# Optimization experiments

Measured on AMD Instinct MI355X. Metric: run time of the kernel, lower is better.

## Reference

```python
import math
import jax, jax.numpy as jnp
import numpy as np

ALPHA = 12.0  # agg_alpha
TAU = 0.07


def setup_inputs() -> dict:
    key = jax.random.key(0)
    kq, kk, kqm, kkm = jax.random.split(key, 4)
    B, Lq, O, Lk, D = 64, 32, 128, 256, 128
    q = jax.random.normal(kq, (B, Lq, D), dtype=jnp.float32)
    k = jax.random.normal(kk, (O, Lk, D), dtype=jnp.float32)
    # True = padding token (masked out)
    q_mask = jax.random.bernoulli(kqm, 0.1, (B, Lq))
    k_mask = jax.random.bernoulli(kkm, 0.1, (O, Lk))
    logit_scale = jnp.asarray(math.log(1.0 / TAU), dtype=jnp.float32)
    return {"q": q, "k": k, "q_mask": q_mask, "k_mask": k_mask,
            "logit_scale": logit_scale}


def _l2norm(x, eps=1e-12):
    # torch F.normalize: x / max(||x||_2, eps)
    n = jnp.sqrt(jnp.sum(x * x, axis=-1, keepdims=True))
    return x / jnp.maximum(n, eps)


def reference(q, k, q_mask, k_mask, logit_scale):
    B, Lq, D = q.shape
    O, Lk, _ = k.shape
    qn = _l2norm(q)
    kn = _l2norm(k)
    # S: [B, O, Lq, Lk] full similarity tensor (the kernel-headroom intermediate)
    S = jnp.einsum('bid,ojd->boij', qn, kn)
    m = q_mask[:, None, :, None] | k_mask[None, :, None, :]
    S = jnp.where(m, -jnp.inf, S)
    # softmax-pool over Lk: logsumexp(alpha*S)/alpha, then sum over Lq
    s = jax.nn.logsumexp(ALPHA * S, axis=-1) / ALPHA  # [B, O, Lq]
    s = jnp.sum(s, axis=-1)                            # [B, O]
    s = jnp.where(jnp.isfinite(s), s, jnp.zeros_like(s))
    # length_norm = 'sqrt'
    s = s / (math.sqrt(Lq * Lk) + 1e-06)
    # learnable temperature, exp clamped at 100
    scale = jnp.minimum(jnp.exp(logit_scale), 100.0)
    return s * scale
```

## Files before the change

### kernel.cpp

```cpp
#include <hip/hip_runtime.h>
#include <math.h>


#define ALPHA 12.0f

constexpr int B_  = 64;
constexpr int LQ  = 32;
constexpr int O_  = 128;
constexpr int LK  = 256;
constexpr int LKH = 128;
constexpr int D_  = 128;
constexpr int LDH = D_ + 8;

typedef _Float16 half8   __attribute__((ext_vector_type(8)));
typedef _Float16 half4_t __attribute__((ext_vector_type(4)));
typedef float    f32x4   __attribute__((ext_vector_type(4)));

__global__ __launch_bounds__(256, 1)
void colbert_partial_kernel(const float* __restrict__ q,
                            const float* __restrict__ k,
                            const int*  __restrict__ q_mask,
                            const int*  __restrict__ k_mask,
                            float* __restrict__ ws)
{
    __shared__ _Float16 kl[LKH][LDH];
    __shared__ _Float16 ql2[2][LQ][LDH];
    __shared__ float rk[LKH];
    __shared__ float bjs[LKH];
    __shared__ float rqa2[2][LQ];
    __shared__ float part2[2][2][LQ];
    __shared__ int   lbm[B_ + 1];

    const int o     = blockIdx.x >> 1;
    const int h     = blockIdx.x & 1;
    const int t     = threadIdx.x;
    const int lane  = t & 63;
    const int w     = t >> 6;
    const int row16 = lane & 15;
    const int quad  = lane >> 4;

    if (w == 0) {
        const int4* qm4 = (const int4*)q_mask;
        int4 mm[8];
        #pragma unroll
        for (int u = 0; u < 8; ++u)
            mm[u] = qm4[lane * 8 + u];
        int any = 0;
        #pragma unroll
        for (int u = 0; u < 8; ++u)
            any |= mm[u].x | mm[u].y | mm[u].z | mm[u].w;
        const bool live = (any == 0);
        unsigned long long mb = __ballot(live);
        if (live) {
            int rank = __popcll(mb & ((1ull << lane) - 1ull));
            lbm[1 + rank] = lane;
        }
        if (lane == 0) lbm[0] = (int)__popcll(mb);
    }

    const float4* kg = (const float4*)(k + ((size_t)o * LK + (size_t)h * LKH) * D_);
    float4 kv[16];
    #pragma unroll
    for (int r = 0; r < 16; ++r)
        kv[r] = kg[t + 256 * r];
    const int km = (t < LKH) ? k_mask[o * LK + h * LKH + t] : 0;

    #pragma unroll
    for (int r = 0; r < 16; ++r) {
        int idx = t + 256 * r;
        int j = idx >> 5, c4 = idx & 31;
        half4_t hh;
        hh[0] = (_Float16)kv[r].x; hh[1] = (_Float16)kv[r].y;
        hh[2] = (_Float16)kv[r].z; hh[3] = (_Float16)kv[r].w;
        *(half4_t*)&kl[j][c4 * 4] = hh;
    }
    __syncthreads();

    const int M = lbm[0];
    if (M == 0) return;

    int midx = 0;
    bool first = true;
    while (midx < M) {
        const int  b0     = lbm[1 + midx];
        const bool has_b1 = (midx + 1 < M);
        const int  b1     = lbm[1 + (has_b1 ? midx + 1 : midx)];
        midx += 2;

        const float4* qg0 = (const float4*)(q + (size_t)b0 * LQ * D_);
        const float4* qg1 = (const float4*)(q + (size_t)b1 * LQ * D_);
        float4 qv0[4], qv1[4];
        #pragma unroll
        for (int r = 0; r < 4; ++r) {
            qv0[r] = qg0[t + 256 * r];
            qv1[r] = qg1[t + 256 * r];
        }

        if (first) {
            if (t < LKH) {
                float ss = 0.f;
                #pragma unroll
                for (int p = 0; p < 16; ++p) {
                    half8 hh = *(const half8*)&kl[t][p * 8];
                    #pragma unroll
                    for (int e = 0; e < 8; ++e) {
                        float x = (float)hh[e];
                        ss = fmaf(x, x, ss);
                    }
                }
                rk[t]  = 1.0f / fmaxf(sqrtf(ss), 1e-12f);
                bjs[t] = (km != 0) ? -1e30f : 0.0f;
            }
            first = false;
        }

        #pragma unroll
        for (int r = 0; r < 4; ++r) {
            int idx = t + 256 * r;
            int i = idx >> 5, c4 = idx & 31;
            half4_t h0, h1;
            h0[0] = (_Float16)qv0[r].x; h0[1] = (_Float16)qv0[r].y;
            h0[2] = (_Float16)qv0[r].z; h0[3] = (_Float16)qv0[r].w;
            h1[0] = (_Float16)qv1[r].x; h1[1] = (_Float16)qv1[r].y;
            h1[2] = (_Float16)qv1[r].z; h1[3] = (_Float16)qv1[r].w;
            *(half4_t*)&ql2[0][i][c4 * 4] = h0;
            *(half4_t*)&ql2[1][i][c4 * 4] = h1;
        }
        __syncthreads();

        if (t < 64) {
            const int pb = t >> 5, i = t & 31;
            float ss = 0.f;
            #pragma unroll
            for (int p = 0; p < 16; ++p) {
                half8 hh = *(const half8*)&ql2[pb][i][p * 8];
                #pragma unroll
                for (int e = 0; e < 8; ++e) {
                    float x = (float)hh[e];
                    ss = fmaf(x, x, ss);
                }
            }
            rqa2[pb][i] = ALPHA / fmaxf(sqrtf(ss), 1e-12f);
        }
        __syncthreads();

        const int i0 = (w >> 1) * 16;
        const int j0 = (w & 1) * 64;

        half8 afrag[2][4];
        #pragma unroll
        for (int pb = 0; pb < 2; ++pb)
            #pragma unroll
            for (int kk = 0; kk < 4; ++kk)
                afrag[pb][kk] =
                    *(const half8*)&ql2[pb][i0 + row16][kk * 32 + quad * 8];

        float rqv[2][4];
        #pragma unroll
        for (int pb = 0; pb < 2; ++pb)
            #pragma unroll
            for (int rg = 0; rg < 4; ++rg)
                rqv[pb][rg] = rqa2[pb][i0 + quad * 4 + rg];

        float esum[2][4] = {{0.f,0.f,0.f,0.f},{0.f,0.f,0.f,0.f}};
        #pragma unroll
        for (int c = 0; c < 4; ++c) {
            const int jt = j0 + c * 16;
            f32x4 acc0 = {0.f, 0.f, 0.f, 0.f};
            f32x4 acc1 = {0.f, 0.f, 0.f, 0.f};
            #pragma unroll
            for (int kk = 0; kk < 4; ++kk) {
                half8 bfrag =
                    *(const half8*)&kl[jt + row16][kk * 32 + quad * 8];
                acc0 = __builtin_amdgcn_mfma_f32_16x16x32_f16(
                           afrag[0][kk], bfrag, acc0, 0, 0, 0);
                acc1 = __builtin_amdgcn_mfma_f32_16x16x32_f16(
                           afrag[1][kk], bfrag, acc1, 0, 0, 0);
            }
            const float rkj = rk[jt + row16];
            const float bb  = bjs[jt + row16];
            #pragma unroll
            for (int rg = 0; rg < 4; ++rg) {
                esum[0][rg] += __expf(acc0[rg] * rqv[0][rg] * rkj + bb);
                esum[1][rg] += __expf(acc1[rg] * rqv[1][rg] * rkj + bb);
            }
        }
        #pragma unroll
        for (int pb = 0; pb < 2; ++pb) {
            #pragma unroll
            for (int rg = 0; rg < 4; ++rg) {
                float e = esum[pb][rg];
                e += __shfl_xor(e, 1);
                e += __shfl_xor(e, 2);
                e += __shfl_xor(e, 4);
                e += __shfl_xor(e, 8);
                esum[pb][rg] = e;
            }
            if (row16 == 0)
                #pragma unroll
                for (int rg = 0; rg < 4; ++rg)
                    part2[pb][w & 1][i0 + quad * 4 + rg] = esum[pb][rg];
        }
        __syncthreads();

        if (t < 64) {
            const int pb = t >> 5, i = t & 31;
            if (pb == 0 || has_b1) {
                const int b = pb ? b1 : b0;
                const float s = part2[pb][0][i] + part2[pb][1][i];
                ws[(((size_t)h * B_ + b) * O_ + o) * LQ + i] = s;
            }
        }
    }
}

__global__ __launch_bounds__(256, 1)
void colbert_finalize_kernel(const float* __restrict__ ws,
                             const int*  __restrict__ q_mask,
                             const float* __restrict__ logit_scale,
                             float* __restrict__ out)
{
    const int t    = threadIdx.x;
    const int lane = t & 63;
    const int w    = t >> 6;
    const int pb   = lane >> 5;
    const int i    = lane & 31;

    const float ls     = logit_scale[0];
    const float scale  = fminf(__expf(ls), 100.0f);
    const float inv_ln = 1.0f / (sqrtf((float)(LQ * LK)) + 1e-6f);
    const int   gw     = blockIdx.x * 4 + w;

    #pragma unroll
    for (int it = 0; it < 4; ++it) {
        const int p = it * 2048 + gw * 2 + pb;
        const int b = p >> 7;
        const int o = p & 127;

        const float s0 = ws[(((size_t)0 * B_ + b) * O_ + o) * LQ + i];
        const float s1 = ws[(((size_t)1 * B_ + b) * O_ + o) * LQ + i];
        const int   qm = q_mask[b * LQ + i];

        const float s = s0 + s1;
        const bool  badrow = (s <= 0.f);
        float tot = __logf(fmaxf(s, 1e-38f));
        tot += __shfl_xor(tot, 16);
        tot += __shfl_xor(tot, 8);
        tot += __shfl_xor(tot, 4);
        tot += __shfl_xor(tot, 2);
        tot += __shfl_xor(tot, 1);

        unsigned long long zb = __ballot(badrow);
        unsigned long long qb = __ballot(qm != 0);
        if (i == 0) {
            unsigned long long half_mask =
                pb ? 0xFFFFFFFF00000000ull : 0x00000000FFFFFFFFull;
            float res = 0.f;
            if (((zb | qb) & half_mask) == 0ull)
                res = (tot * (1.0f / ALPHA)) * inv_ln * scale;
            out[b * O_ + o] = res;
        }
    }
}

extern "C" void kernel_launch(void* const* d_in, const int* in_sizes, int n_in,
                              void* d_out, int out_size, void* d_ws, size_t ws_size,
                              hipStream_t stream) {
    const float* q           = (const float*)d_in[0];
    const float* k           = (const float*)d_in[1];
    const int*   q_mask      = (const int*)d_in[2];
    const int*   k_mask      = (const int*)d_in[3];
    const float* logit_scale = (const float*)d_in[4];
    float* out = (float*)d_out;
    float* ws  = (float*)d_ws;

    colbert_partial_kernel<<<O_ * 2, 256, 0, stream>>>(q, k, q_mask, k_mask, ws);
    colbert_finalize_kernel<<<256, 256, 0, stream>>>(ws, q_mask, logit_scale, out);
}
```

Measured before the change: 79.09 us.

## Split Lk into four slices and fuse partial and finalize via cooperative grid sync

Each key object's 256 tokens are now split across four blocks instead of two, giving 512 blocks with launch bounds raised to two blocks per CU. The partial and finalize phases are fused into one cooperative kernel with a grid-wide sync, replacing the second kernel launch. The finalize step now sums four partial slices from the workspace. If the cooperative launch fails, it falls back to two separate launches. The trade-off is more workspace traffic, a grid barrier, and the query loads and normalisation being repeated across twice as many blocks.

```diff
diff --git a/kernel.cpp b/kernel.cpp
--- a/kernel.cpp
+++ b/kernel.cpp
@@ -1,5 +1,8 @@
 #include <hip/hip_runtime.h>
+#include <hip/hip_cooperative_groups.h>
 #include <math.h>
+
+namespace cg = cooperative_groups;
 
 
 #define ALPHA 12.0f
@@ -8,20 +11,22 @@
 constexpr int LQ  = 32;
 constexpr int O_  = 128;
 constexpr int LK  = 256;
-constexpr int LKH = 128;
+constexpr int NH  = 4;
+constexpr int LKH = LK / NH;
 constexpr int D_  = 128;
 constexpr int LDH = D_ + 8;
+constexpr int GRID = O_ * NH;
 
 typedef _Float16 half8   __attribute__((ext_vector_type(8)));
 typedef _Float16 half4_t __attribute__((ext_vector_type(4)));
 typedef float    f32x4   __attribute__((ext_vector_type(4)));
 
-__global__ __launch_bounds__(256, 1)
-void colbert_partial_kernel(const float* __restrict__ q,
-                            const float* __restrict__ k,
-                            const int*  __restrict__ q_mask,
-                            const int*  __restrict__ k_mask,
-                            float* __restrict__ ws)
+__device__ __forceinline__
+void partial_phase(const float* __restrict__ q,
+                   const float* __restrict__ k,
+                   const int*  __restrict__ q_mask,
+                   const int*  __restrict__ k_mask,
+                   float* __restrict__ ws)
 {
     __shared__ _Float16 kl[LKH][LDH];
     __shared__ _Float16 ql2[2][LQ][LDH];
@@ -31,8 +36,8 @@
     __shared__ float part2[2][2][LQ];
     __shared__ int   lbm[B_ + 1];
 
-    const int o     = blockIdx.x >> 1;
-    const int h     = blockIdx.x & 1;
+    const int o     = blockIdx.x >> 2;
+    const int h     = blockIdx.x & 3;
     const int t     = threadIdx.x;
     const int lane  = t & 63;
     const int w     = t >> 6;
@@ -59,14 +64,14 @@
     }
 
     const float4* kg = (const float4*)(k + ((size_t)o * LK + (size_t)h * LKH) * D_);
-    float4 kv[16];
+    float4 kv[8];
     #pragma unroll
-    for (int r = 0; r < 16; ++r)
+    for (int r = 0; r < 8; ++r)
         kv[r] = kg[t + 256 * r];
     const int km = (t < LKH) ? k_mask[o * LK + h * LKH + t] : 0;
 
     #pragma unroll
-    for (int r = 0; r < 16; ++r) {
+    for (int r = 0; r < 8; ++r) {
         int idx = t + 256 * r;
         int j = idx >> 5, c4 = idx & 31;
         half4_t hh;
@@ -77,148 +82,148 @@
     __syncthreads();
 
     const int M = lbm[0];
-    if (M == 0) return;
-
-    int midx = 0;
-    bool first = true;
-    while (midx < M) {
-        const int  b0     = lbm[1 + midx];
-        const bool has_b1 = (midx + 1 < M);
-        const int  b1     = lbm[1 + (has_b1 ? midx + 1 : midx)];
-        midx += 2;
-
-        const float4* qg0 = (const float4*)(q + (size_t)b0 * LQ * D_);
-        const float4* qg1 = (const float4*)(q + (size_t)b1 * LQ * D_);
-        float4 qv0[4], qv1[4];
-        #pragma unroll
-        for (int r = 0; r < 4; ++r) {
-            qv0[r] = qg0[t + 256 * r];
-            qv1[r] = qg1[t + 256 * r];
-        }
-
-        if (first) {
-            if (t < LKH) {
+    if (M > 0) {
+        int midx = 0;
+        bool first = true;
+        while (midx < M) {
+            const int  b0     = lbm[1 + midx];
+            const bool has_b1 = (midx + 1 < M);
+            const int  b1     = lbm[1 + (has_b1 ? midx + 1 : midx)];
+            midx += 2;
+
+            const float4* qg0 = (const float4*)(q + (size_t)b0 * LQ * D_);
+            const float4* qg1 = (const float4*)(q + (size_t)b1 * LQ * D_);
+            float4 qv0[4], qv1[4];
+            #pragma unroll
+            for (int r = 0; r < 4; ++r) {
+                qv0[r] = qg0[t + 256 * r];
+                qv1[r] = qg1[t + 256 * r];
+            }
+
+            if (first) {
+                if (t < LKH) {
+                    float ss = 0.f;
+                    #pragma unroll
+                    for (int p = 0; p < 16; ++p) {
+                        half8 hh = *(const half8*)&kl[t][p * 8];
+                        #pragma unroll
+                        for (int e = 0; e < 8; ++e) {
+                            float x = (float)hh[e];
+                            ss = fmaf(x, x, ss);
+                        }
+                    }
+                    rk[t]  = 1.0f / fmaxf(sqrtf(ss), 1e-12f);
+                    bjs[t] = (km != 0) ? -1e30f : 0.0f;
+                }
+                first = false;
+            }
+
+            #pragma unroll
+            for (int r = 0; r < 4; ++r) {
+                int idx = t + 256 * r;
+                int i = idx >> 5, c4 = idx & 31;
+                half4_t h0, h1;
+                h0[0] = (_Float16)qv0[r].x; h0[1] = (_Float16)qv0[r].y;
+                h0[2] = (_Float16)qv0[r].z; h0[3] = (_Float16)qv0[r].w;
+                h1[0] = (_Float16)qv1[r].x; h1[1] = (_Float16)qv1[r].y;
+                h1[2] = (_Float16)qv1[r].z; h1[3] = (_Float16)qv1[r].w;
+                *(half4_t*)&ql2[0][i][c4 * 4] = h0;
+                *(half4_t*)&ql2[1][i][c4 * 4] = h1;
+            }
+            __syncthreads();
+
+            if (t < 64) {
+                const int pb = t >> 5, i = t & 31;
                 float ss = 0.f;
                 #pragma unroll
                 for (int p = 0; p < 16; ++p) {
-                    half8 hh = *(const half8*)&kl[t][p * 8];
+                    half8 hh = *(const half8*)&ql2[pb][i][p * 8];
                     #pragma unroll
                     for (int e = 0; e < 8; ++e) {
                         float x = (float)hh[e];
                         ss = fmaf(x, x, ss);
                     }
                 }
-                rk[t]  = 1.0f / fmaxf(sqrtf(ss), 1e-12f);
-                bjs[t] = (km != 0) ? -1e30f : 0.0f;
-            }
-            first = false;
+                rqa2[pb][i] = ALPHA / fmaxf(sqrtf(ss), 1e-12f);
+            }
+            __syncthreads();
+
+            const int i0 = (w >> 1) * 16;
+            const int j0 = (w & 1) * 32;
+
+            half8 afrag[2][4];
+            #pragma unroll
+            for (int pb = 0; pb < 2; ++pb)
+                #pragma unroll
+                for (int kk = 0; kk < 4; ++kk)
+                    afrag[pb][kk] =
+                        *(const half8*)&ql2[pb][i0 + row16][kk * 32 + quad * 8];
+
+            float rqv[2][4];
+            #pragma unroll
+            for (int pb = 0; pb < 2; ++pb)
+                #pragma unroll
+                for (int rg = 0; rg < 4; ++rg)
+                    rqv[pb][rg] = rqa2[pb][i0 + quad * 4 + rg];
+
+            float esum[2][4] = {{0.f,0.f,0.f,0.f},{0.f,0.f,0.f,0.f}};
+            #pragma unroll
+            for (int c = 0; c < 2; ++c) {
+                const int jt = j0 + c * 16;
+                f32x4 acc0 = {0.f, 0.f, 0.f, 0.f};
+                f32x4 acc1 = {0.f, 0.f, 0.f, 0.f};
+                #pragma unroll
+                for (int kk = 0; kk < 4; ++kk) {
+                    half8 bfrag =
+                        *(const half8*)&kl[jt + row16][kk * 32 + quad * 8];
+                    acc0 = __builtin_amdgcn_mfma_f32_16x16x32_f16(
+                               afrag[0][kk], bfrag, acc0, 0, 0, 0);
+                    acc1 = __builtin_amdgcn_mfma_f32_16x16x32_f16(
+                               afrag[1][kk], bfrag, acc1, 0, 0, 0);
+                }
+                const float rkj = rk[jt + row16];
+                const float bb  = bjs[jt + row16];
+                #pragma unroll
+                for (int rg = 0; rg < 4; ++rg) {
+                    esum[0][rg] += __expf(acc0[rg] * rqv[0][rg] * rkj + bb);
+                    esum[1][rg] += __expf(acc1[rg] * rqv[1][rg] * rkj + bb);
+                }
+            }
+            #pragma unroll
+            for (int pb = 0; pb < 2; ++pb) {
+                #pragma unroll
+                for (int rg = 0; rg < 4; ++rg) {
+                    float e = esum[pb][rg];
+                    e += __shfl_xor(e, 1);
+                    e += __shfl_xor(e, 2);
+                    e += __shfl_xor(e, 4);
+                    e += __shfl_xor(e, 8);
+                    esum[pb][rg] = e;
+                }
+                if (row16 == 0)
+                    #pragma unroll
+                    for (int rg = 0; rg < 4; ++rg)
+                        part2[pb][w & 1][i0 + quad * 4 + rg] = esum[pb][rg];
+            }
+            __syncthreads();
+
+            if (t < 64) {
+                const int pb = t >> 5, i = t & 31;
+                if (pb == 0 || has_b1) {
+                    const int b = pb ? b1 : b0;
+                    const float s = part2[pb][0][i] + part2[pb][1][i];
+                    ws[(((size_t)h * B_ + b) * O_ + o) * LQ + i] = s;
+                }
+            }
         }
-
-        #pragma unroll
-        for (int r = 0; r < 4; ++r) {
-            int idx = t + 256 * r;
-            int i = idx >> 5, c4 = idx & 31;
-            half4_t h0, h1;
-            h0[0] = (_Float16)qv0[r].x; h0[1] = (_Float16)qv0[r].y;
-            h0[2] = (_Float16)qv0[r].z; h0[3] = (_Float16)qv0[r].w;
-            h1[0] = (_Float16)qv1[r].x; h1[1] = (_Float16)qv1[r].y;
-            h1[2] = (_Float16)qv1[r].z; h1[3] = (_Float16)qv1[r].w;
-            *(half4_t*)&ql2[0][i][c4 * 4] = h0;
-            *(half4_t*)&ql2[1][i][c4 * 4] = h1;
-        }
-        __syncthreads();
-
-        if (t < 64) {
-            const int pb = t >> 5, i = t & 31;
-            float ss = 0.f;
-            #pragma unroll
-            for (int p = 0; p < 16; ++p) {
-                half8 hh = *(const half8*)&ql2[pb][i][p * 8];
-                #pragma unroll
-                for (int e = 0; e < 8; ++e) {
-                    float x = (float)hh[e];
-                    ss = fmaf(x, x, ss);
-                }
-            }
-            rqa2[pb][i] = ALPHA / fmaxf(sqrtf(ss), 1e-12f);
-        }
-        __syncthreads();
-
-        const int i0 = (w >> 1) * 16;
-        const int j0 = (w & 1) * 64;
-
-        half8 afrag[2][4];
-        #pragma unroll
-        for (int pb = 0; pb < 2; ++pb)
-            #pragma unroll
-            for (int kk = 0; kk < 4; ++kk)
-                afrag[pb][kk] =
-                    *(const half8*)&ql2[pb][i0 + row16][kk * 32 + quad * 8];
-
-        float rqv[2][4];
-        #pragma unroll
-        for (int pb = 0; pb < 2; ++pb)
-            #pragma unroll
-            for (int rg = 0; rg < 4; ++rg)
-                rqv[pb][rg] = rqa2[pb][i0 + quad * 4 + rg];
-
-        float esum[2][4] = {{0.f,0.f,0.f,0.f},{0.f,0.f,0.f,0.f}};
-        #pragma unroll
-        for (int c = 0; c < 4; ++c) {
-            const int jt = j0 + c * 16;
-            f32x4 acc0 = {0.f, 0.f, 0.f, 0.f};
-            f32x4 acc1 = {0.f, 0.f, 0.f, 0.f};
-            #pragma unroll
-            for (int kk = 0; kk < 4; ++kk) {
-                half8 bfrag =
-                    *(const half8*)&kl[jt + row16][kk * 32 + quad * 8];
-                acc0 = __builtin_amdgcn_mfma_f32_16x16x32_f16(
-                           afrag[0][kk], bfrag, acc0, 0, 0, 0);
-                acc1 = __builtin_amdgcn_mfma_f32_16x16x32_f16(
-                           afrag[1][kk], bfrag, acc1, 0, 0, 0);
-            }
-            const float rkj = rk[jt + row16];
-            const float bb  = bjs[jt + row16];
-            #pragma unroll
-            for (int rg = 0; rg < 4; ++rg) {
-                esum[0][rg] += __expf(acc0[rg] * rqv[0][rg] * rkj + bb);
-                esum[1][rg] += __expf(acc1[rg] * rqv[1][rg] * rkj + bb);
-            }
-        }
-        #pragma unroll
-        for (int pb = 0; pb < 2; ++pb) {
-            #pragma unroll
-            for (int rg = 0; rg < 4; ++rg) {
-                float e = esum[pb][rg];
-                e += __shfl_xor(e, 1);
-                e += __shfl_xor(e, 2);
-                e += __shfl_xor(e, 4);
-                e += __shfl_xor(e, 8);
-                esum[pb][rg] = e;
-            }
-            if (row16 == 0)
-                #pragma unroll
-                for (int rg = 0; rg < 4; ++rg)
-                    part2[pb][w & 1][i0 + quad * 4 + rg] = esum[pb][rg];
-        }
-        __syncthreads();
-
-        if (t < 64) {
-            const int pb = t >> 5, i = t & 31;
-            if (pb == 0 || has_b1) {
-                const int b = pb ? b1 : b0;
-                const float s = part2[pb][0][i] + part2[pb][1][i];
-                ws[(((size_t)h * B_ + b) * O_ + o) * LQ + i] = s;
-            }
-        }
-    }
-}
-
-__global__ __launch_bounds__(256, 1)
-void colbert_finalize_kernel(const float* __restrict__ ws,
-                             const int*  __restrict__ q_mask,
-                             const float* __restrict__ logit_scale,
-                             float* __restrict__ out)
+    }
+}
+
+__device__ __forceinline__
+void finalize_phase(const float* __restrict__ ws,
+                    const int*  __restrict__ q_mask,
+                    const float* __restrict__ logit_scale,
+                    float* __restrict__ out)
 {
     const int t    = threadIdx.x;
     const int lane = t & 63;
@@ -232,16 +237,17 @@
     const int   gw     = blockIdx.x * 4 + w;
 
     #pragma unroll
-    for (int it = 0; it < 4; ++it) {
-        const int p = it * 2048 + gw * 2 + pb;
+    for (int it = 0; it < 2; ++it) {
+        const int p = it * 4096 + gw * 2 + pb;
         const int b = p >> 7;
         const int o = p & 127;
 
-        const float s0 = ws[(((size_t)0 * B_ + b) * O_ + o) * LQ + i];
-        const float s1 = ws[(((size_t)1 * B_ + b) * O_ + o) * LQ + i];
-        const int   qm = q_mask[b * LQ + i];
-
-        const float s = s0 + s1;
+        float s = 0.f;
+        #pragma unroll
+        for (int hh = 0; hh < NH; ++hh)
+            s += ws[(((size_t)hh * B_ + b) * O_ + o) * LQ + i];
+        const int qm = q_mask[b * LQ + i];
+
         const bool  badrow = (s <= 0.f);
         float tot = __logf(fmaxf(s, 1e-38f));
         tot += __shfl_xor(tot, 16);
@@ -263,6 +269,40 @@
     }
 }
 
+__global__ __launch_bounds__(256, 2)
+void colbert_coop_kernel(const float* __restrict__ q,
+                         const float* __restrict__ k,
+                         const int*  __restrict__ q_mask,
+                         const int*  __restrict__ k_mask,
+                         const float* __restrict__ logit_scale,
+                         float* __restrict__ ws,
+                         float* __restrict__ out)
+{
+    partial_phase(q, k, q_mask, k_mask, ws);
+    __threadfence();
+    cg::this_grid().sync();
+    finalize_phase(ws, q_mask, logit_scale, out);
+}
+
+__global__ __launch_bounds__(256, 2)
+void colbert_partial_kernel(const float* __restrict__ q,
+                            const float* __restrict__ k,
+                            const int*  __restrict__ q_mask,
+                            const int*  __restrict__ k_mask,
+                            float* __restrict__ ws)
+{
+    partial_phase(q, k, q_mask, k_mask, ws);
+}
+
+__global__ __launch_bounds__(256, 2)
+void colbert_finalize_kernel(const float* __restrict__ ws,
+                             const int*  __restrict__ q_mask,
+                             const float* __restrict__ logit_scale,
+                             float* __restrict__ out)
+{
+    finalize_phase(ws, q_mask, logit_scale, out);
+}
+
 extern "C" void kernel_launch(void* const* d_in, const int* in_sizes, int n_in,
                               void* d_out, int out_size, void* d_ws, size_t ws_size,
                               hipStream_t stream) {
@@ -274,6 +314,13 @@
     float* out = (float*)d_out;
     float* ws  = (float*)d_ws;
 
-    colbert_partial_kernel<<<O_ * 2, 256, 0, stream>>>(q, k, q_mask, k_mask, ws);
-    colbert_finalize_kernel<<<256, 256, 0, stream>>>(ws, q_mask, logit_scale, out);
-}
+    void* args[7] = {(void*)&q, (void*)&k, (void*)&q_mask, (void*)&k_mask,
+                     (void*)&logit_scale, (void*)&ws, (void*)&out};
+    hipError_t e = hipLaunchCooperativeKernel(
+        (const void*)colbert_coop_kernel, dim3(GRID), dim3(256),
+        args, 0, stream);
+    if (e != hipSuccess) {
+        colbert_partial_kernel<<<GRID, 256, 0, stream>>>(q, k, q_mask, k_mask, ws);
+        colbert_finalize_kernel<<<GRID, 256, 0, stream>>>(ws, q_mask, logit_scale, out);
+    }
+}
```

Measured after the change: 185.8 us. 2.35x slower.
